# Kernel tuning notes

Hardware: AMD Instinct MI355X
Metric: run time of the kernel (lower is better)

## Reference

```python
import jax, jax.numpy as jnp
import numpy as np

B, C_IN, K = 32, 512, 1024
C_MID, C_OUT, N_CLS = 128, 64, 5
SIGMA, ADJ_RATIO = 2.0, 0.2
KEEP_TOP, DROP_P = 0.2, 0.5
NUM_TOP = int(max(KEEP_TOP * K + 1, 1))            # 205
NUM_REST = K - NUM_TOP
NUM_DROP = int(max(NUM_REST * DROP_P + 0.5, 1))    # 410
NUM_KEPT = int(max(NUM_REST - NUM_DROP, 1))        # 409
DROP_SCALE = 1.0 - float(NUM_DROP) / K
ADJ_K = max(int(ADJ_RATIO * K), 1)
EPS = 1e-8


def setup_inputs() -> dict:
    key = jax.random.key(0)
    ks = jax.random.split(key, 8)
    return {
        "x": jax.random.normal(ks[0], (B, C_IN, K), jnp.float32),
        "importances_batch": jax.random.uniform(ks[1], (B, 1, K), jnp.float32),
        "random_mask": jax.random.uniform(ks[2], (B, K), jnp.float32),
        "W1": jax.random.normal(ks[3], (C_IN, C_MID), jnp.float32) / np.sqrt(C_IN),
        "W2": jax.random.normal(ks[4], (C_MID, C_OUT), jnp.float32) / np.sqrt(C_MID),
        "fc_w": jax.random.normal(ks[5], (C_OUT, N_CLS), jnp.float32) / np.sqrt(C_OUT),
        "id_w": jax.random.normal(ks[6], (C_IN, C_OUT), jnp.float32) / np.sqrt(C_IN),
        "id_b": jnp.zeros((C_OUT,), jnp.float32),
    }


def _scatter_mask(idx):  # idx [B, n] -> one-hot-union mask [B, K]
    rows = jnp.arange(B)[:, None]
    return jnp.zeros((B, K), jnp.float32).at[rows, idx].set(1.0)


def _sga_masks(imp, rand_mask):
    # imp [B,1,K] -> detached masks (stop_gradient mirrors .detach())
    imp_f = jax.lax.stop_gradient(imp[:, 0, :])
    rand_mask = jax.lax.stop_gradient(rand_mask)
    top_idx = jax.lax.top_k(imp_f, NUM_TOP)[1]
    top = _scatter_mask(top_idx)
    rm1 = jnp.where(top > 0, -10.0, rand_mask)
    kept = _scatter_mask(jax.lax.top_k(rm1, NUM_KEPT)[1])
    rm2 = jnp.where(top > 0, 10.0, rand_mask)
    drop = _scatter_mask(jax.lax.top_k(-rm2, NUM_DROP)[1])  # ascending sort head
    return top[:, None, :], kept[:, None, :], drop[:, None, :]


def _adj_prior(imp):
    d = imp[:, 0, :, None] - imp[:, 0, None, :]           # [B,K,K]
    A = jnp.exp(-(d * d) / (2.0 * SIGMA * SIGMA))
    A = A + jnp.eye(K, dtype=A.dtype)                      # self loop
    return A / (A.sum(-1, keepdims=True) + EPS)


def _adj_feature(feat):
    # feat [B,C,K]: row top-k thresholded cosine similarity
    n = feat / (jnp.linalg.norm(feat, axis=1, keepdims=True) + EPS)
    sim = jnp.einsum('bck,bcj->bkj', n, n)                 # [B,K,K]
    thr = jax.lax.top_k(sim, ADJ_K)[0][..., -1:]
    A = jnp.where(sim >= thr, sim, 0.0)
    A = A + jnp.eye(K, dtype=A.dtype)
    return A / (A.sum(-1, keepdims=True) + EPS)


def _gcl(feat, W, adjs):
    h = jnp.einsum('bck,co->bok', feat, W)                 # per-node linear
    s = sum(jnp.einsum('bok,bkj->boj', h, A) for A in adjs)
    return jax.nn.relu(s)


def reference(x, importances_batch, random_mask, W1, W2, fc_w, id_w, id_b):
    imp = importances_batch
    top, kept, drop = _sga_masks(imp, random_mask)
    batch_mask = top + kept  # disjoint supports

    adjP = _adj_prior(imp)
    adjF1 = _adj_feature(x)
    emb1 = _gcl(x, W1, [adjP, adjF1])                      # [B,C_MID,K]
    adjF2 = _adj_feature(emb1)

    emb1_kept = emb1 * jnp.clip(top + kept, 0.0, 1.0) / DROP_SCALE
    bag_kept = jnp.sum(emb1_kept * imp, axis=-1)
    emb2_kept = _gcl(emb1_kept, W2, [adjP, adjF2])
    emb1_drop = emb1 * jnp.clip(top + drop, 0.0, 1.0) / DROP_SCALE
    bag_drop = jnp.sum(emb1_drop * imp, axis=-1)
    emb2 = emb2_kept * batch_mask

    bag = jnp.sum(emb2 * imp, axis=-1)                     # [B,C_OUT]
    pooled_x = jnp.sum(x * imp, axis=-1)                   # [B,C_IN]
    ident = jax.nn.relu(pooled_x @ id_w + id_b)
    output = (bag + ident) @ fc_w                          # [B,N_CLS]
    return output, emb1, bag_kept, bag_drop
```

## Files before the change

kernel.cpp:

```cpp
#include <hip/hip_runtime.h>
#include <hip/hip_bf16.h>
#include <math.h>

#define BN_ 32
#define CIN 512
#define KN 1024
#define CMID 128
#define COUT 64
#define NCLS 5
#define NUM_TOP 205
#define NUM_KEPT 409
#define NUM_DROP 410
#define ADJ_KK 204
#define EPSF 1e-8f
#define INV_DS (1.0f / 0.599609375f)

typedef __bf16 bf16x8 __attribute__((ext_vector_type(8)));
typedef float f32x4 __attribute__((ext_vector_type(4)));

__device__ inline ushort f2bf(float x) {
  union { __hip_bfloat16 b; ushort u; } c;
  c.b = __float2bfloat16(x);
  return c.u;
}

__device__ inline void gll16(const ushort* g, ushort* l) {
  __builtin_amdgcn_global_load_lds(
      (const __attribute__((address_space(1))) unsigned int*)g,
      (__attribute__((address_space(3))) unsigned int*)l, 16, 0, 0);
}

__global__ __launch_bounds__(256) void maskpsum_kernel(const float* __restrict__ imp,
                                                       float* __restrict__ topM,
                                                       float* __restrict__ invSumP) {
  int b = blockIdx.y;
  int t = threadIdx.x;
  int io = t >> 2;
  int part = t & 3;
  int i = blockIdx.x * 64 + io;
  __shared__ float im[KN];
  for (int j = t; j < KN; j += 256) im[j] = imp[(size_t)b * KN + j];
  __syncthreads();
  float vi = im[i];
  int j0 = part * 256;
  int rank = 0;
  float s = 0.0f;
#pragma unroll 4
  for (int jj = 0; jj < 256; ++jj) {
    int j = j0 + jj;
    float a = im[j];
    rank += (a > vi || (a == vi && j < i)) ? 1 : 0;
    float d = vi - a;
    s += __expf(-d * d * 0.125f);
  }
  rank += __shfl_xor(rank, 1);
  rank += __shfl_xor(rank, 2);
  s += __shfl_xor(s, 1);
  s += __shfl_xor(s, 2);
  if (part == 0) {
    topM[(size_t)b * KN + i] = (rank < NUM_TOP) ? 1.0f : 0.0f;
    invSumP[(size_t)b * KN + i] = 1.0f / (s + 1.0f + EPSF);
  }
}

__global__ __launch_bounds__(256) void masks2_kernel(const float* __restrict__ rnd,
                                                     const float* __restrict__ topM,
                                                     float* __restrict__ mTK,
                                                     float* __restrict__ mTD) {
  int b = blockIdx.y;
  int t = threadIdx.x;
  int io = t >> 2;
  int part = t & 3;
  int i = blockIdx.x * 64 + io;
  __shared__ float r1s[KN];
  __shared__ float r2s[KN];
  for (int j = t; j < KN; j += 256) {
    float tv = topM[(size_t)b * KN + j];
    float rv = rnd[(size_t)b * KN + j];
    r1s[j] = (tv > 0.5f) ? -10.0f : rv;
    r2s[j] = (tv > 0.5f) ? 10.0f : rv;
  }
  __syncthreads();
  float v1 = r1s[i];
  float v2 = r2s[i];
  int j0 = part * 256;
  int c1 = 0, c2 = 0;
#pragma unroll 4
  for (int jj = 0; jj < 256; ++jj) {
    int j = j0 + jj;
    float a = r1s[j];
    float bb2 = r2s[j];
    c1 += (a > v1 || (a == v1 && j < i)) ? 1 : 0;
    c2 += (bb2 < v2 || (bb2 == v2 && j < i)) ? 1 : 0;
  }
  c1 += __shfl_xor(c1, 1);
  c1 += __shfl_xor(c1, 2);
  c2 += __shfl_xor(c2, 1);
  c2 += __shfl_xor(c2, 2);
  if (part == 0) {
    int top = topM[(size_t)b * KN + i] > 0.5f;
    mTK[(size_t)b * KN + i] = (top || c1 < NUM_KEPT) ? 1.0f : 0.0f;
    mTD[(size_t)b * KN + i] = (top || c2 < NUM_DROP) ? 1.0f : 0.0f;
  }
}

template <int C>
__global__ void colnorm_kernel(const float* __restrict__ f, float* __restrict__ inv,
                               float* __restrict__ nrm) {
  int idx = blockIdx.x * 256 + threadIdx.x;
  int b = idx >> 10;
  int k = idx & (KN - 1);
  const float* fb = f + (size_t)b * C * KN + k;
  float ss = 0.0f;
  for (int c = 0; c < C; ++c) {
    float v = fb[(size_t)c * KN];
    ss += v * v;
  }
  float n = sqrtf(ss) + EPSF;
  inv[idx] = 1.0f / n;
  nrm[idx] = n;
}

template <int R, int CC>
__global__ __launch_bounds__(256) void wtrans_kernel(const float* __restrict__ W,
                                                     ushort* __restrict__ WT) {
  int idx = blockIdx.x * 256 + threadIdx.x;
  int o = idx / R;
  int c = idx - o * R;
  WT[(size_t)o * R + c] = f2bf(W[(size_t)c * CC + o]);
}

template <int C>
__global__ void xpose_kernel(const float* __restrict__ f, const float* __restrict__ inv,
                             __hip_bfloat16* __restrict__ oT, int bstart) {
  int brel = blockIdx.z;
  int b = bstart + brel;
  int k0 = blockIdx.x * 64;
  int c0 = blockIdx.y * 64;
  __shared__ float t[64][65];
  const float* fb = f + (size_t)b * C * KN;
  int tx = threadIdx.x & 63;
  int ty = threadIdx.x >> 6;
  for (int r = 0; r < 64; r += 4) t[r + ty][tx] = fb[(size_t)(c0 + r + ty) * KN + k0 + tx];
  __syncthreads();
  __hip_bfloat16* ob = oT + (size_t)brel * KN * C;
  for (int r = 0; r < 64; r += 4) {
    int k = r + ty;
    float s = inv[(size_t)b * KN + k0 + k];
    ob[(size_t)(k0 + k) * C + c0 + tx] = __float2bfloat16(t[tx][k] * s);
  }
}

template <int C>
__global__ __launch_bounds__(256) void simf_kernel(const ushort* __restrict__ xT,
                                                   float* __restrict__ sim, int nb) {
  int f = blockIdx.x;
  int brel, tile;
  if ((nb & 7) == 0) {
    int xcd = f & 7;
    int wdx = f >> 3;
    brel = xcd * (nb >> 3) + (wdx >> 6);
    tile = wdx & 63;
  } else {
    brel = f >> 6;
    tile = f & 63;
  }
  int t = threadIdx.x;
  int lane = t & 63;
  int wid = t >> 6;
  int iB = (tile >> 3) * 128;
  int jB = (tile & 7) * 128;
  const ushort* X = xT + (size_t)brel * KN * C;

  __shared__ ushort smem[16384];
  ushort* AsB = smem;
  ushort* BsB = smem + 8192;

  int srow = t >> 2;
  int scol = (((t & 3) ^ ((t >> 3) & 3))) * 8;
  int ldst = t * 8;

  auto stage = [&](int bufi, int c0) {
    gll16(X + (size_t)(iB + srow) * C + c0 + scol, &AsB[bufi * 4096 + ldst]);
    gll16(X + (size_t)(iB + 64 + srow) * C + c0 + scol, &AsB[bufi * 4096 + 2048 + ldst]);
    gll16(X + (size_t)(jB + srow) * C + c0 + scol, &BsB[bufi * 4096 + ldst]);
    gll16(X + (size_t)(jB + 64 + srow) * C + c0 + scol, &BsB[bufi * 4096 + 2048 + ldst]);
  };

  int i0loc = (wid >> 1) * 64;
  int j0loc = (wid & 1) * 64;
  int r = lane & 15;
  int sseg = lane >> 4;

  f32x4 acc[4][4] = {};
  stage(0, 0);
  __syncthreads();
  constexpr int NT = C / 32;
  int cur = 0;
#pragma unroll 2
  for (int ks = 0; ks < NT; ++ks) {
    if (ks + 1 < NT) stage(cur ^ 1, (ks + 1) * 32);
    bf16x8 a[4], bb[4];
#pragma unroll
    for (int m = 0; m < 4; ++m) {
      int row = i0loc + m * 16 + r;
      int off = row * 32 + ((sseg ^ ((row >> 1) & 3)) << 3);
      a[m] = *reinterpret_cast<const bf16x8*>(&AsB[cur * 4096 + off]);
    }
#pragma unroll
    for (int n = 0; n < 4; ++n) {
      int row = j0loc + n * 16 + r;
      int off = row * 32 + ((sseg ^ ((row >> 1) & 3)) << 3);
      bb[n] = *reinterpret_cast<const bf16x8*>(&BsB[cur * 4096 + off]);
    }
#pragma unroll
    for (int m = 0; m < 4; ++m)
#pragma unroll
      for (int n = 0; n < 4; ++n)
        acc[m][n] = __builtin_amdgcn_mfma_f32_16x16x32_bf16(a[m], bb[n], acc[m][n], 0, 0, 0);
    __syncthreads();
    cur ^= 1;
  }

  float(*buf)[65] = (float(*)[65])((float*)smem + (size_t)wid * 16 * 65);
  int orow = (lane >> 4) * 4;
  int ocol = lane & 15;
  int i0 = iB + i0loc;
  int j0 = jB + j0loc;
  ushort* simb = (ushort*)sim + (size_t)brel * KN * 2048;
#pragma unroll
  for (int m = 0; m < 4; ++m) {
#pragma unroll
    for (int n = 0; n < 4; ++n)
#pragma unroll
      for (int rr = 0; rr < 4; ++rr) buf[orow + rr][n * 16 + ocol] = acc[m][n][rr];
#pragma unroll
    for (int rr = 0; rr < 4; ++rr) {
      int row = rr * 4 + (lane >> 4);
      float4 v4 = *(const float4*)&buf[row][(lane & 15) * 4];
      ushort4 r4;
      r4.x = f2bf(v4.x);
      r4.y = f2bf(v4.y);
      r4.z = f2bf(v4.z);
      r4.w = f2bf(v4.w);
      *(ushort4*)(simb + (size_t)(i0 + m * 16 + row) * 2048 + j0 + (lane & 15) * 4) = r4;
    }
  }
}

__global__ __launch_bounds__(256) void thrfin_kernel(float* __restrict__ A,
                                                     const float* __restrict__ imp,
                                                     const float* __restrict__ invSumP,
                                                     int bstart) {
  int brel = blockIdx.y;
  int b = bstart + brel;
  int wid = threadIdx.x >> 6;
  int lane = threadIdx.x & 63;
  int i = blockIdx.x * 4 + wid;
  ushort* row = (ushort*)A + ((size_t)brel * KN + i) * 2048;
  __shared__ float im[KN];
  ((float4*)im)[threadIdx.x] = ((const float4*)(imp + (size_t)b * KN))[threadIdx.x];
  __syncthreads();

  ushort4 v[4];
  unsigned key[16];
#pragma unroll
  for (int q = 0; q < 4; ++q) v[q] = ((const ushort4*)row)[lane + 64 * q];
#pragma unroll
  for (int q = 0; q < 4; ++q) {
    const ushort* pv = (const ushort*)&v[q];
#pragma unroll
    for (int e = 0; e < 4; ++e) {
      ushort u = pv[e];
      key[q * 4 + e] = (u & 0x8000u) ? (unsigned)(ushort)~u : (unsigned)(u | 0x8000u);
    }
  }
  unsigned tk = 0u;
#pragma unroll 1
  for (int bit = 15; bit >= 0; --bit) {
    unsigned cand = tk | (1u << bit);
    int c = 0;
#pragma unroll
    for (int e = 0; e < 8; ++e)
      c += (int)__popcll(__ballot(key[e] >= cand));
    int cl = 0;
#pragma unroll
    for (int e = 8; e < 16; ++e) cl += (key[e] >= cand) ? 1 : 0;
#pragma unroll
    for (int off = 32; off > 0; off >>= 1) cl += __shfl_xor(cl, off);
    c += cl;
    if (c >= ADJ_KK) tk = cand;
  }
  float m[16];
  float s = 0.0f;
#pragma unroll
  for (int q = 0; q < 4; ++q) {
    const ushort* pv = (const ushort*)&v[q];
#pragma unroll
    for (int e = 0; e < 4; ++e) {
      float val = __uint_as_float(((unsigned)pv[e]) << 16);
      float mv = (key[q * 4 + e] >= tk) ? val : 0.0f;
      m[q * 4 + e] = mv;
      s += mv;
    }
  }
#pragma unroll
  for (int off = 32; off > 0; off >>= 1) s += __shfl_xor(s, off);
  float invF = 1.0f / (s + 1.0f + EPSF);
  float vi = im[i];
  float invP = invSumP[(size_t)b * KN + i];
#pragma unroll
  for (int q = 0; q < 4; ++q) {
    float4 iv = ((const float4*)im)[lane + 64 * q];
    const float* ip = (const float*)&iv;
    ushort4 r;
    ushort* rp = (ushort*)&r;
    int colb = 4 * lane + 256 * q;
#pragma unroll
    for (int e = 0; e < 4; ++e) {
      float diag = (colb + e == i) ? 1.0f : 0.0f;
      float d = vi - ip[e];
      rp[e] = f2bf((m[q * 4 + e] + diag) * invF + (__expf(-d * d * 0.125f) + diag) * invP);
    }
    ((ushort4*)row)[lane + 64 * q] = r;
  }
}

__global__ __launch_bounds__(256) void at_kernel(float* __restrict__ Asim) {
  int brel = blockIdx.z;
  int k0 = blockIdx.x * 64;
  int j0 = blockIdx.y * 64;
  __shared__ ushort t[64][68];
  ushort* Ab = (ushort*)(Asim + (size_t)brel * KN * KN);
  int g = threadIdx.x & 15;
  int r = threadIdx.x >> 4;
#pragma unroll
  for (int p = 0; p < 4; ++p) {
    int row = p * 16 + r;
    *(ushort4*)&t[row][g * 4] =
        *(const ushort4*)&Ab[(size_t)(k0 + row) * 2048 + j0 + g * 4];
  }
  __syncthreads();
#pragma unroll
  for (int p = 0; p < 4; ++p) {
    int j = p * 16 + r;
    ushort4 v;
    v.x = t[g * 4 + 0][j];
    v.y = t[g * 4 + 1][j];
    v.z = t[g * 4 + 2][j];
    v.w = t[g * 4 + 3][j];
    *(ushort4*)&Ab[(size_t)(j0 + j) * 2048 + 1024 + k0 + g * 4] = v;
  }
}

template <int C, bool MASK>
__global__ __launch_bounds__(256) void linf_kernel(const ushort* __restrict__ xg,
                                                   const ushort* __restrict__ WT,
                                                   const float* __restrict__ nrm,
                                                   const float* __restrict__ mTK,
                                                   ushort* __restrict__ hg, int M,
                                                   int bstart) {
  int brel = blockIdx.z;
  int b = bstart + brel;
  int t = threadIdx.x;
  int lane = t & 63;
  int wid = t >> 6;
  int iB = blockIdx.y * 64;
  int jB = blockIdx.x * 128;
  const ushort* xb = xg + (size_t)brel * KN * C;

  __shared__ ushort smem[12288];
  ushort* HsB = smem;
  ushort* BsB = smem + 4096;

  int srow = t >> 2;
  int scol = (t & 3) * 8;
  int ldst = t * 8;

  auto stage = [&](int bufi, int c0) {
    gll16(WT + (size_t)(iB + srow) * C + c0 + scol, &HsB[bufi * 2048 + ldst]);
    gll16(xb + (size_t)(jB + srow) * C + c0 + scol, &BsB[bufi * 4096 + ldst]);
    gll16(xb + (size_t)(jB + 64 + srow) * C + c0 + scol, &BsB[bufi * 4096 + 2048 + ldst]);
  };

  int i0loc = (wid >> 1) * 32;
  int j0loc = (wid & 1) * 64;
  int r = lane & 15;
  int s = (lane >> 4) * 8;

  f32x4 acc[2][4] = {};
  stage(0, 0);
  __syncthreads();
  int cur = 0;
#pragma unroll 2
  for (int ks = 0; ks < C / 32; ++ks) {
    if (ks + 1 < C / 32) stage(cur ^ 1, (ks + 1) * 32);
    bf16x8 a[2], bb[4];
#pragma unroll
    for (int m = 0; m < 2; ++m)
      a[m] = *reinterpret_cast<const bf16x8*>(&HsB[cur * 2048 + (i0loc + m * 16 + r) * 32 + s]);
#pragma unroll
    for (int n = 0; n < 4; ++n)
      bb[n] = *reinterpret_cast<const bf16x8*>(&BsB[cur * 4096 + (j0loc + n * 16 + r) * 32 + s]);
#pragma unroll
    for (int m = 0; m < 2; ++m)
#pragma unroll
      for (int n = 0; n < 4; ++n)
        acc[m][n] = __builtin_amdgcn_mfma_f32_16x16x32_bf16(a[m], bb[n], acc[m][n], 0, 0, 0);
    __syncthreads();
    cur ^= 1;
  }

  float(*buf)[65] = (float(*)[65])((float*)smem + (size_t)wid * 16 * 65);
  int orow = (lane >> 4) * 4;
  int ocol = lane & 15;
  int i0 = iB + i0loc;
  int j0 = jB + j0loc;
#pragma unroll
  for (int m = 0; m < 2; ++m) {
#pragma unroll
    for (int n = 0; n < 4; ++n)
#pragma unroll
      for (int rr = 0; rr < 4; ++rr) buf[orow + rr][n * 16 + ocol] = acc[m][n][rr];
#pragma unroll
    for (int rr = 0; rr < 4; ++rr) {
      int row = rr * 4 + (lane >> 4);
      int kk = j0 + (lane & 15) * 4;
      float4 v4 = *(const float4*)&buf[row][(lane & 15) * 4];
      float4 nv = *(const float4*)(nrm + (size_t)b * KN + kk);
      float f0 = nv.x, f1 = nv.y, f2 = nv.z, f3 = nv.w;
      if (MASK) {
        float4 mv = *(const float4*)(mTK + (size_t)b * KN + kk);
        f0 *= mv.x * INV_DS;
        f1 *= mv.y * INV_DS;
        f2 *= mv.z * INV_DS;
        f3 *= mv.w * INV_DS;
      }
      ushort4 r4;
      r4.x = f2bf(v4.x * f0);
      r4.y = f2bf(v4.y * f1);
      r4.z = f2bf(v4.z * f2);
      r4.w = f2bf(v4.w * f3);
      *(ushort4*)(hg + ((size_t)brel * M + i0 + m * 16 + row) * KN + kk) = r4;
    }
  }
}

template <int M, bool LOCAL>
__global__ __launch_bounds__(256) void sgemmf_kernel(const ushort* __restrict__ hB,
                                                     const float* __restrict__ Asim,
                                                     float* __restrict__ outp, int bstart) {
  int brel = blockIdx.z;
  int b = bstart + brel;
  int t = threadIdx.x;
  int lane = t & 63;
  int wid = t >> 6;
  int iB = blockIdx.y * 64;
  int jB = blockIdx.x * 128;
  const ushort* hb = hB + (size_t)(LOCAL ? brel : b) * M * KN;
  const ushort* Ab = (const ushort*)(Asim + (size_t)brel * KN * KN);

  __shared__ ushort smem[12288];
  ushort* HsB = smem;
  ushort* BsB = smem + 4096;

  int srow = t >> 2;
  int scol = (t & 3) * 8;
  int ldst = t * 8;

  auto stage = [&](int bufi, int k0) {
    gll16(hb + (size_t)(iB + srow) * KN + k0 + scol, &HsB[bufi * 2048 + ldst]);
    gll16(Ab + (size_t)(jB + srow) * 2048 + 1024 + k0 + scol, &BsB[bufi * 4096 + ldst]);
    gll16(Ab + (size_t)(jB + 64 + srow) * 2048 + 1024 + k0 + scol,
          &BsB[bufi * 4096 + 2048 + ldst]);
  };

  int i0loc = (wid >> 1) * 32;
  int j0loc = (wid & 1) * 64;
  int r = lane & 15;
  int s = (lane >> 4) * 8;

  f32x4 acc[2][4] = {};
  stage(0, 0);
  __syncthreads();
  int cur = 0;
#pragma unroll 2
  for (int ks = 0; ks < KN / 32; ++ks) {
    if (ks + 1 < KN / 32) stage(cur ^ 1, (ks + 1) * 32);
    bf16x8 a[2], bb[4];
#pragma unroll
    for (int m = 0; m < 2; ++m)
      a[m] = *reinterpret_cast<const bf16x8*>(&HsB[cur * 2048 + (i0loc + m * 16 + r) * 32 + s]);
#pragma unroll
    for (int n = 0; n < 4; ++n)
      bb[n] = *reinterpret_cast<const bf16x8*>(&BsB[cur * 4096 + (j0loc + n * 16 + r) * 32 + s]);
#pragma unroll
    for (int m = 0; m < 2; ++m)
#pragma unroll
      for (int n = 0; n < 4; ++n)
        acc[m][n] = __builtin_amdgcn_mfma_f32_16x16x32_bf16(a[m], bb[n], acc[m][n], 0, 0, 0);
    __syncthreads();
    cur ^= 1;
  }

  float(*buf)[65] = (float(*)[65])((float*)smem + (size_t)wid * 16 * 65);
  int orow = (lane >> 4) * 4;
  int ocol = lane & 15;
  int i0 = iB + i0loc;
  int j0 = jB + j0loc;
  float* ob = outp + (size_t)b * M * KN;
#pragma unroll
  for (int m = 0; m < 2; ++m) {
#pragma unroll
    for (int n = 0; n < 4; ++n)
#pragma unroll
      for (int rr = 0; rr < 4; ++rr) buf[orow + rr][n * 16 + ocol] = fmaxf(acc[m][n][rr], 0.0f);
#pragma unroll
    for (int rr = 0; rr < 4; ++rr) {
      int row = rr * 4 + (lane >> 4);
      float4 v4 = *(const float4*)&buf[row][(lane & 15) * 4];
      *(float4*)(ob + (size_t)(i0 + m * 16 + row) * KN + j0 + (lane & 15) * 4) = v4;
    }
  }
}

__global__ void bag12_kernel(const float* __restrict__ emb1, const float* __restrict__ mTK,
                             const float* __restrict__ mTD, const float* __restrict__ imp,
                             float* __restrict__ bagk, float* __restrict__ bagd) {
  int c = blockIdx.x, b = blockIdx.y;
  int t = threadIdx.x;
  const float* e = emb1 + ((size_t)b * CMID + c) * KN;
  const float* ir = imp + (size_t)b * KN;
  const float* m1 = mTK + (size_t)b * KN;
  const float* m2 = mTD + (size_t)b * KN;
  float s1 = 0.0f, sd = 0.0f;
  for (int k = t; k < KN; k += 256) {
    float ev = e[k] * ir[k];
    s1 += ev * m1[k];
    sd += ev * m2[k];
  }
  __shared__ float r1[256], r2[256];
  r1[t] = s1;
  r2[t] = sd;
  __syncthreads();
  for (int st = 128; st > 0; st >>= 1) {
    if (t < st) {
      r1[t] += r1[t + st];
      r2[t] += r2[t + st];
    }
    __syncthreads();
  }
  if (t == 0) {
    bagk[(size_t)b * CMID + c] = r1[0] * INV_DS;
    bagd[(size_t)b * CMID + c] = r2[0] * INV_DS;
  }
}

__global__ void bag2_kernel(const float* __restrict__ s2, const float* __restrict__ mTK,
                            const float* __restrict__ imp, float* __restrict__ bag) {
  int o = blockIdx.x, b = blockIdx.y;
  int t = threadIdx.x;
  const float* sr = s2 + ((size_t)b * COUT + o) * KN;
  const float* ir = imp + (size_t)b * KN;
  const float* mr = mTK + (size_t)b * KN;
  float s = 0.0f;
  for (int k = t; k < KN; k += 256) s += sr[k] * mr[k] * ir[k];
  __shared__ float red[256];
  red[t] = s;
  __syncthreads();
  for (int st = 128; st > 0; st >>= 1) {
    if (t < st) red[t] += red[t + st];
    __syncthreads();
  }
  if (t == 0) bag[(size_t)b * COUT + o] = red[0];
}

__global__ void pooled_kernel(const float* __restrict__ x, const float* __restrict__ imp,
                              float* __restrict__ pooled) {
  int c = blockIdx.x, b = blockIdx.y;
  int t = threadIdx.x;
  const float* xr = x + (size_t)(b * CIN + c) * KN;
  const float* ir = imp + (size_t)b * KN;
  float s = 0.0f;
  for (int k = t; k < KN; k += 256) s += xr[k] * ir[k];
  __shared__ float red[256];
  red[t] = s;
  __syncthreads();
  for (int st = 128; st > 0; st >>= 1) {
    if (t < st) red[t] += red[t + st];
    __syncthreads();
  }
  if (t == 0) pooled[(size_t)b * CIN + c] = red[0];
}

__global__ void final_kernel(const float* __restrict__ pooled, const float* __restrict__ bag,
                             const float* __restrict__ id_w, const float* __restrict__ id_b,
                             const float* __restrict__ fc_w, float* __restrict__ out) {
  int b = blockIdx.x;
  int o = threadIdx.x;
  __shared__ float v[COUT];
  float s = id_b[o];
  const float* pr = pooled + (size_t)b * CIN;
  for (int c = 0; c < CIN; ++c) s += pr[c] * id_w[(size_t)c * COUT + o];
  v[o] = bag[(size_t)b * COUT + o] + fmaxf(s, 0.0f);
  __syncthreads();
  if (o < NCLS) {
    float acc = 0.0f;
    for (int oo = 0; oo < COUT; ++oo) acc += v[oo] * fc_w[(size_t)oo * NCLS + o];
    out[(size_t)b * NCLS + o] = acc;
  }
}

extern "C" void kernel_launch(void* const* d_in, const int* in_sizes, int n_in,
                              void* d_out, int out_size, void* d_ws, size_t ws_size,
                              hipStream_t stream) {
  const float* x = (const float*)d_in[0];
  const float* imp = (const float*)d_in[1];
  const float* rnd = (const float*)d_in[2];
  const float* W1 = (const float*)d_in[3];
  const float* W2 = (const float*)d_in[4];
  const float* fc_w = (const float*)d_in[5];
  const float* id_w = (const float*)d_in[6];
  const float* id_b = (const float*)d_in[7];
  float* out = (float*)d_out;
  float* emb1 = out + BN_ * NCLS;
  float* bagk = emb1 + (size_t)BN_ * CMID * KN;
  float* bagd = bagk + (size_t)BN_ * CMID;

  float* w = (float*)d_ws;
  size_t off = 0;
  auto take = [&](size_t n) {
    float* p = w + off;
    off += n;
    return p;
  };
  float* invSumP = take((size_t)BN_ * KN);
  float* invNX = take((size_t)BN_ * KN);
  float* invNE = take((size_t)BN_ * KN);
  float* nrmX = take((size_t)BN_ * KN);
  float* nrmE = take((size_t)BN_ * KN);
  float* topM = take((size_t)BN_ * KN);
  float* mTK = take((size_t)BN_ * KN);
  float* mTD = take((size_t)BN_ * KN);
  float* bag = take((size_t)BN_ * COUT);
  float* pooled = take((size_t)BN_ * CIN);
  ushort* W1T = (ushort*)take((size_t)CMID * CIN / 2);
  ushort* W2T = (ushort*)take((size_t)COUT * CMID / 2);

  const size_t s2_f = (size_t)BN_ * COUT * KN;
  const size_t xg1 = (size_t)CIN * KN / 2;
  const size_t hg1 = (size_t)CMID * KN / 2;
  const size_t eg1 = (size_t)CMID * KN / 2;
  const size_t hg2_1 = (size_t)COUT * KN / 2;

  size_t budget = ws_size / 4;
  int nb = 1;
  const int cands[6] = {32, 16, 8, 4, 2, 1};
  for (int ci = 0; ci < 6; ++ci) {
    size_t c = cands[ci];
    size_t uA = c * (xg1 + hg1);
    size_t uB = s2_f + c * (eg1 + hg2_1);
    size_t uMax = uA > uB ? uA : uB;
    if (off + uMax + c * (size_t)KN * KN <= budget) {
      nb = (int)c;
      break;
    }
  }
  size_t uA = (size_t)nb * (xg1 + hg1);
  size_t uB = s2_f + (size_t)nb * (eg1 + hg2_1);
  float* U = take(uA > uB ? uA : uB);
  ushort* xnT = (ushort*)U;
  ushort* h = (ushort*)(U + (size_t)nb * xg1);
  ushort* enT = (ushort*)U;
  ushort* h2 = (ushort*)(U + (size_t)nb * eg1);
  float* s2 = U + (size_t)nb * (eg1 + hg2_1);
  float* simA = take((size_t)nb * KN * KN);

  maskpsum_kernel<<<dim3(KN / 64, BN_), 256, 0, stream>>>(imp, topM, invSumP);
  masks2_kernel<<<dim3(KN / 64, BN_), 256, 0, stream>>>(rnd, topM, mTK, mTD);
  colnorm_kernel<CIN><<<(BN_ * KN) / 256, 256, 0, stream>>>(x, invNX, nrmX);
  wtrans_kernel<CIN, CMID><<<(CMID * CIN) / 256, 256, 0, stream>>>(W1, W1T);
  wtrans_kernel<CMID, COUT><<<(COUT * CMID) / 256, 256, 0, stream>>>(W2, W2T);

  for (int bs = 0; bs < BN_; bs += nb) {
    xpose_kernel<CIN><<<dim3(KN / 64, CIN / 64, nb), 256, 0, stream>>>(
        x, invNX, (__hip_bfloat16*)xnT, bs);
    linf_kernel<CIN, false><<<dim3(KN / 128, CMID / 64, nb), 256, 0, stream>>>(
        xnT, W1T, nrmX, nullptr, h, CMID, bs);
    simf_kernel<CIN><<<nb * 64, 256, 0, stream>>>(xnT, simA, nb);
    thrfin_kernel<<<dim3(KN / 4, nb), 256, 0, stream>>>(simA, imp, invSumP, bs);
    at_kernel<<<dim3(KN / 64, KN / 64, nb), 256, 0, stream>>>(simA);
    sgemmf_kernel<CMID, true><<<dim3(KN / 128, CMID / 64, nb), 256, 0, stream>>>(h, simA, emb1,
                                                                                 bs);
  }

  colnorm_kernel<CMID><<<(BN_ * KN) / 256, 256, 0, stream>>>(emb1, invNE, nrmE);

  for (int bs = 0; bs < BN_; bs += nb) {
    xpose_kernel<CMID><<<dim3(KN / 64, CMID / 64, nb), 256, 0, stream>>>(
        emb1, invNE, (__hip_bfloat16*)enT, bs);
    linf_kernel<CMID, true><<<dim3(KN / 128, COUT / 64, nb), 256, 0, stream>>>(
        enT, W2T, nrmE, mTK, h2, COUT, bs);
    simf_kernel<CMID><<<nb * 64, 256, 0, stream>>>(enT, simA, nb);
    thrfin_kernel<<<dim3(KN / 4, nb), 256, 0, stream>>>(simA, imp, invSumP, bs);
    at_kernel<<<dim3(KN / 64, KN / 64, nb), 256, 0, stream>>>(simA);
    sgemmf_kernel<COUT, true><<<dim3(KN / 128, COUT / 64, nb), 256, 0, stream>>>(h2, simA, s2,
                                                                                 bs);
  }

  bag12_kernel<<<dim3(CMID, BN_), 256, 0, stream>>>(emb1, mTK, mTD, imp, bagk, bagd);
  bag2_kernel<<<dim3(COUT, BN_), 256, 0, stream>>>(s2, mTK, imp, bag);
  pooled_kernel<<<dim3(CIN, BN_), 256, 0, stream>>>(x, imp, pooled);
  final_kernel<<<BN_, 64, 0, stream>>>(pooled, bag, id_w, id_b, fc_w, out);
}
```

Baseline: 418.3 us.

## Exploit Gram matrix symmetry: compute upper-triangle tiles, mirror-store transposes

The cosine-similarity kernel now launches only the 36 upper-triangular 128x128 tiles per batch instead of all 64. Each off-diagonal tile also writes its transpose into the mirrored position through an XOR-swizzled shared-memory staging buffer. This removes nearly half of the similarity GEMM MFMA work and operand loads. In exchange it adds extra shared-memory transposes and syncs, and drops the previous XCD-aware block-to-batch mapping.

Result: no change. 423.5 us (+1.2%).

```diff
diff --git a/kernel.cpp b/kernel.cpp
--- a/kernel.cpp
+++ b/kernel.cpp
@@ -154,22 +154,21 @@
 template <int C>
 __global__ __launch_bounds__(256) void simf_kernel(const ushort* __restrict__ xT,
                                                    float* __restrict__ sim, int nb) {
+  (void)nb;
   int f = blockIdx.x;
-  int brel, tile;
-  if ((nb & 7) == 0) {
-    int xcd = f & 7;
-    int wdx = f >> 3;
-    brel = xcd * (nb >> 3) + (wdx >> 6);
-    tile = wdx & 63;
-  } else {
-    brel = f >> 6;
-    tile = f & 63;
-  }
+  int brel = f / 36;
+  int rem = f - brel * 36;
+  int ti = 0;
+  while (rem >= 8 - ti) {
+    rem -= 8 - ti;
+    ++ti;
+  }
+  int tj = ti + rem;
   int t = threadIdx.x;
   int lane = t & 63;
   int wid = t >> 6;
-  int iB = (tile >> 3) * 128;
-  int jB = (tile & 7) * 128;
+  int iB = ti * 128;
+  int jB = tj * 128;
   const ushort* X = xT + (size_t)brel * KN * C;
 
   __shared__ ushort smem[16384];
@@ -244,6 +243,35 @@
       r4.z = f2bf(v4.z);
       r4.w = f2bf(v4.w);
       *(ushort4*)(simb + (size_t)(i0 + m * 16 + row) * 2048 + j0 + (lane & 15) * 4) = r4;
+    }
+  }
+
+  if (iB != jB) {
+    __syncthreads();
+    ushort* Tm = smem;
+#pragma unroll
+    for (int m = 0; m < 4; ++m)
+#pragma unroll
+      for (int n = 0; n < 4; ++n) {
+        int cu = ((i0loc + m * 16) >> 2) + (lane >> 4);
+        int row = j0loc + n * 16 + (lane & 15);
+        int u = cu ^ (row & 15);
+        ushort4 val;
+        val.x = f2bf(acc[m][n][0]);
+        val.y = f2bf(acc[m][n][1]);
+        val.z = f2bf(acc[m][n][2]);
+        val.w = f2bf(acc[m][n][3]);
+        *(ushort4*)&Tm[row * 128 + u * 4] = val;
+      }
+    __syncthreads();
+    int row = t >> 1;
+    int half = t & 1;
+    ushort* dstrow = simb + (size_t)(jB + row) * 2048 + iB;
+#pragma unroll
+    for (int k = 0; k < 16; ++k) {
+      int cu = half * 16 + k;
+      int u = cu ^ (row & 15);
+      *(ushort4*)(dstrow + cu * 4) = *(const ushort4*)&Tm[row * 128 + u * 4];
     }
   }
 }
@@ -687,7 +715,7 @@
         x, invNX, (__hip_bfloat16*)xnT, bs);
     linf_kernel<CIN, false><<<dim3(KN / 128, CMID / 64, nb), 256, 0, stream>>>(
         xnT, W1T, nrmX, nullptr, h, CMID, bs);
-    simf_kernel<CIN><<<nb * 64, 256, 0, stream>>>(xnT, simA, nb);
+    simf_kernel<CIN><<<nb * 36, 256, 0, stream>>>(xnT, simA, nb);
     thrfin_kernel<<<dim3(KN / 4, nb), 256, 0, stream>>>(simA, imp, invSumP, bs);
     at_kernel<<<dim3(KN / 64, KN / 64, nb), 256, 0, stream>>>(simA);
     sgemmf_kernel<CMID, true><<<dim3(KN / 128, CMID / 64, nb), 256, 0, stream>>>(h, simA, emb1,
@@ -701,7 +729,7 @@
         emb1, invNE, (__hip_bfloat16*)enT, bs);
     linf_kernel<CMID, true><<<dim3(KN / 128, COUT / 64, nb), 256, 0, stream>>>(
         enT, W2T, nrmE, mTK, h2, COUT, bs);
-    simf_kernel<CMID><<<nb * 64, 256, 0, stream>>>(enT, simA, nb);
+    simf_kernel<CMID><<<nb * 36, 256, 0, stream>>>(enT, simA, nb);
     thrfin_kernel<<<dim3(KN / 4, nb), 256, 0, stream>>>(simA, imp, invSumP, bs);
     at_kernel<<<dim3(KN / 64, KN / 64, nb), 256, 0, stream>>>(simA);
     sgemmf_kernel<COUT, true><<<dim3(KN / 128, COUT / 64, nb), 256, 0, stream>>>(h2, simA, s2,
```
